# Performance work log

Hardware: AMD Instinct MI355X
Metric: run time of the kernel (lower is better)

The kernel has to match this reference:

```python
import jax, jax.numpy as jnp
import numpy as np
from jax import lax

N_QUBITS = 4


def _apply_ry(state, wire, theta):
    """Apply RY(theta) on `wire`. state: [N,2,2,2,2] real. theta: scalar or [N]."""
    theta = jnp.asarray(theta)
    if theta.ndim == 1:
        theta = theta.reshape(-1, 1, 1, 1)  # broadcast over remaining qubit axes
    s = jnp.moveaxis(state, 1 + wire, -1)
    c, sn = jnp.cos(theta / 2), jnp.sin(theta / 2)
    s0, s1 = s[..., 0], s[..., 1]
    s = jnp.stack([c * s0 - sn * s1, sn * s0 + c * s1], axis=-1)
    return jnp.moveaxis(s, -1, 1 + wire)


def _apply_cnot(state, ctrl, tgt):
    s = jnp.moveaxis(state, (1 + ctrl, 1 + tgt), (-2, -1))
    s = s.at[..., 1, :].set(s[..., 1, ::-1])
    return jnp.moveaxis(s, (-2, -1), (1 + ctrl, 1 + tgt))


def _quantum_filter(patches, angles):
    """patches: [N,4] rotation angles per qubit; returns PauliZ expectations [N,4]."""
    n = patches.shape[0]
    state = jnp.zeros((n, 2, 2, 2, 2), dtype=patches.dtype)
    state = state.at[:, 0, 0, 0, 0].set(1.0)  # |0000>
    # GeneralEncoder: RY(x_i) on wire i
    for w in range(N_QUBITS):
        state = _apply_ry(state, w, patches[:, w])
    # fixed 8-op random layer: 5 RY (learned angles) + 3 CNOTs
    state = _apply_ry(state, 0, angles[0])
    state = _apply_ry(state, 1, angles[1])
    state = _apply_cnot(state, 0, 1)
    state = _apply_ry(state, 2, angles[2])
    state = _apply_cnot(state, 1, 2)
    state = _apply_ry(state, 3, angles[3])
    state = _apply_cnot(state, 2, 3)
    state = _apply_ry(state, 0, angles[4])
    # MeasureAll(PauliZ): <Z_w> = sum probs * (+1/-1 on wire w)
    probs = state * state  # real amplitudes -> |psi|^2
    z = jnp.array([1.0, -1.0], dtype=patches.dtype)
    ez = [
        (probs * z.reshape((1,) + (1,) * w + (2,) + (1,) * (N_QUBITS - 1 - w))).sum(axis=(1, 2, 3, 4))
        for w in range(N_QUBITS)
    ]
    return jnp.stack(ez, axis=-1)  # [N,4]


def setup_inputs() -> dict:
    key = jax.random.key(0)
    ks = jax.random.split(key, 6)
    B = 4096
    return {
        "x": jax.random.normal(ks[0], (B, 1, 28, 28), dtype=jnp.float32),
        "conv_w": jax.random.normal(ks[1], (4, 1, 2, 2), dtype=jnp.float32) * 0.5,
        "conv_b": jax.random.normal(ks[2], (4,), dtype=jnp.float32) * 0.1,
        "angles": jax.random.normal(ks[3], (5,), dtype=jnp.float32) * np.pi,
        "fc_w": jax.random.normal(ks[4], (10, 4 * 14 * 14), dtype=jnp.float32) * 0.03,
        "fc_b": jax.random.normal(ks[5], (10,), dtype=jnp.float32) * 0.1,
    }


def reference(x, conv_w, conv_b, angles, fc_w, fc_b):
    # classical conv: kernel 2, stride 2 -> [B,4,14,14]
    y = lax.conv_general_dilated(
        x, conv_w, window_strides=(2, 2), padding="VALID",
        dimension_numbers=("NCHW", "OIHW", "NCHW"),
    ) + conv_b[None, :, None, None]
    B, C, H, W = y.shape
    patches = y.transpose(0, 2, 3, 1).reshape(B * H * W, C)  # [B*196, 4]
    feats = _quantum_filter(patches, angles)                  # [B*196, 4]
    feats = feats.reshape(B, H * W, C).transpose(0, 2, 1).reshape(B, -1)
    logits = feats @ fc_w.T + fc_b
    return jax.nn.log_softmax(logits, axis=-1)
```

## Files before the change

kernel.cpp:

```cpp
#include <hip/hip_runtime.h>
#include <math.h>

#define NP 196
#define FEAT 784


__device__ __forceinline__ void apply_cnot(float* s, const int mc, const int mt) {
#pragma unroll
    for (int i = 0; i < 16; ++i) {
        if ((i & mc) && !(i & mt)) {
            float t = s[i];
            s[i]      = s[i | mt];
            s[i | mt] = t;
        }
    }
}

__global__ void __launch_bounds__(256)
quanv_fused(const float* __restrict__ x,
            const float* __restrict__ cw,
            const float* __restrict__ cb,
            const float* __restrict__ ang,
            const float* __restrict__ W,
            const float* __restrict__ bias,
            float* __restrict__ out) {
    __shared__ float feats[FEAT];

    const int b   = blockIdx.x;
    const int tid = threadIdx.x;

    if (tid < NP) {
        const int i = tid / 14;
        const int j = tid - i * 14;

        const float* xp = x + b * 784 + (2 * i) * 28 + 2 * j;
        const float2 r0 = *(const float2*)(xp);
        const float2 r1 = *(const float2*)(xp + 28);

        float cs[4], sn[4];
#pragma unroll
        for (int c = 0; c < 4; ++c) {
            float th = cw[c * 4 + 0] * r0.x + cw[c * 4 + 1] * r0.y +
                       cw[c * 4 + 2] * r1.x + cw[c * 4 + 3] * r1.y +
                       (cb[c] + ang[c]);
            __sincosf(0.5f * th, &sn[c], &cs[c]);
        }

        float s[16];
        {
            float v00 = cs[0] * cs[1], v01 = cs[0] * sn[1];
            float v10 = sn[0] * cs[1], v11 = sn[0] * sn[1];
            float w00 = cs[2] * cs[3], w01 = cs[2] * sn[3];
            float w10 = sn[2] * cs[3], w11 = sn[2] * sn[3];
            s[ 0] = v00 * w00; s[ 1] = v00 * w01; s[ 2] = v00 * w10; s[ 3] = v00 * w11;
            s[ 4] = v01 * w00; s[ 5] = v01 * w01; s[ 6] = v01 * w10; s[ 7] = v01 * w11;
            s[ 8] = v10 * w00; s[ 9] = v10 * w01; s[10] = v10 * w10; s[11] = v10 * w11;
            s[12] = v11 * w00; s[13] = v11 * w01; s[14] = v11 * w10; s[15] = v11 * w11;
        }

        apply_cnot(s, 8, 4);
        apply_cnot(s, 4, 2);
        apply_cnot(s, 2, 1);

        float p[16];
#pragma unroll
        for (int idx = 0; idx < 16; ++idx) p[idx] = s[idx] * s[idx];

        float q[8], d[8], xx[8];
#pragma unroll
        for (int jj = 0; jj < 8; ++jj) {
            q[jj]  = p[jj] + p[jj + 8];
            d[jj]  = p[jj] - p[jj + 8];
            xx[jj] = s[jj] * s[jj + 8];
        }

        float A = q[0] + q[1], Bq = q[2] + q[3], C = q[4] + q[5], D = q[6] + q[7];
        float ez1 = (A + Bq) - (C + D);
        float ez2 = (A - Bq) + (C - D);
        float ez3 = (q[0] - q[1]) + (q[2] - q[3]) + (q[4] - q[5]) + (q[6] - q[7]);

        float Dsum = ((d[0] + d[1]) + (d[2] + d[3])) + ((d[4] + d[5]) + (d[6] + d[7]));
        float Xsum = ((xx[0] + xx[1]) + (xx[2] + xx[3])) + ((xx[4] + xx[5]) + (xx[6] + xx[7]));
        float ca4, sa4;
        __sincosf(ang[4], &sa4, &ca4);
        float ez0 = ca4 * Dsum - sa4 * (2.0f * Xsum);

        feats[0 * NP + tid] = ez0;
        feats[1 * NP + tid] = ez1;
        feats[2 * NP + tid] = ez2;
        feats[3 * NP + tid] = ez3;
    }

    __syncthreads();

    if (tid < 64) {
        const int lane = tid;
        float acc[10];
#pragma unroll
        for (int k = 0; k < 10; ++k) acc[k] = 0.f;

        for (int c = lane; c < NP; c += 64) {
            const float4 f = *(const float4*)&feats[c * 4];
            const float* wp = W + c * 4;
#pragma unroll
            for (int k = 0; k < 10; ++k) {
                const float4 w = *(const float4*)(wp + k * FEAT);
                acc[k] += fmaf(f.x, w.x, fmaf(f.y, w.y, fmaf(f.z, w.z, f.w * w.w)));
            }
        }

#pragma unroll
        for (int k = 0; k < 10; ++k) {
#pragma unroll
            for (int off = 32; off > 0; off >>= 1)
                acc[k] += __shfl_down(acc[k], off, 64);
        }

        if (lane == 0) {
            float l[10], m = -INFINITY;
#pragma unroll
            for (int k = 0; k < 10; ++k) {
                l[k] = acc[k] + bias[k];
                m = fmaxf(m, l[k]);
            }
            float ssum = 0.f;
#pragma unroll
            for (int k = 0; k < 10; ++k) ssum += __expf(l[k] - m);
            float ls = __logf(ssum) + m;
            float* o = out + b * 10;
#pragma unroll
            for (int k = 0; k < 10; ++k) o[k] = l[k] - ls;
        }
    }
}

extern "C" void kernel_launch(void* const* d_in, const int* in_sizes, int n_in,
                              void* d_out, int out_size, void* d_ws, size_t ws_size,
                              hipStream_t stream) {
    const float* x      = (const float*)d_in[0];
    const float* conv_w = (const float*)d_in[1];
    const float* conv_b = (const float*)d_in[2];
    const float* angles = (const float*)d_in[3];
    const float* fc_w   = (const float*)d_in[4];
    const float* fc_b   = (const float*)d_in[5];
    float* out = (float*)d_out;

    int B = in_sizes[0] / 784;
    quanv_fused<<<B, 256, 0, stream>>>(x, conv_w, conv_b, angles, fc_w, fc_b, out);
}
```

Measured before the change: 76.61 us.

## Process four images per block so all waves do quantum and FC work

Each 256-thread block now handles four images. All threads compute quantum features for 784 patches, with loads batched up front. Each of the four waves then runs the FC and log-softmax for one image. Previously 60 threads sat idle in the feature stage and three of four waves sat idle in the FC stage; the change raises utilization and cuts the grid size four-fold, at the cost of more registers and shared memory per block.

```diff
diff --git a/kernel.cpp b/kernel.cpp
--- a/kernel.cpp
+++ b/kernel.cpp
@@ -1,8 +1,9 @@
 #include <hip/hip_runtime.h>
 #include <math.h>
 
-#define NP 196
+#define NP   196
 #define FEAT 784
+#define IPB  4
 
 
 __device__ __forceinline__ void apply_cnot(float* s, const int mc, const int mt) {
@@ -16,121 +17,143 @@
     }
 }
 
-__global__ void __launch_bounds__(256)
+__global__ void __launch_bounds__(256, 4)
 quanv_fused(const float* __restrict__ x,
             const float* __restrict__ cw,
             const float* __restrict__ cb,
             const float* __restrict__ ang,
             const float* __restrict__ W,
             const float* __restrict__ bias,
-            float* __restrict__ out) {
-    __shared__ float feats[FEAT];
+            float* __restrict__ out,
+            const int B) {
+    __shared__ float feats[IPB][FEAT];
 
-    const int b   = blockIdx.x;
     const int tid = threadIdx.x;
+    const int b0  = blockIdx.x * IPB;
 
-    if (tid < NP) {
-        const int i = tid / 14;
-        const int j = tid - i * 14;
+    float2 r0v[4], r1v[4];
+#pragma unroll
+    for (int r = 0; r < 4; ++r) {
+        const int p = tid + 256 * r;
+        if (p < IPB * NP) {
+            const int im = p / NP;
+            const int k  = p - im * NP;
+            const int i  = k / 14;
+            const int j  = k - i * 14;
+            int img = b0 + im;
+            if (img >= B) img = B - 1;
+            const float* xp = x + img * 784 + (2 * i) * 28 + 2 * j;
+            r0v[r] = *(const float2*)(xp);
+            r1v[r] = *(const float2*)(xp + 28);
+        }
+    }
 
-        const float* xp = x + b * 784 + (2 * i) * 28 + 2 * j;
-        const float2 r0 = *(const float2*)(xp);
-        const float2 r1 = *(const float2*)(xp + 28);
+#pragma unroll
+    for (int r = 0; r < 4; ++r) {
+        const int p = tid + 256 * r;
+        if (p < IPB * NP) {
+            const int im = p / NP;
+            const int k  = p - im * NP;
+            const float2 r0 = r0v[r];
+            const float2 r1 = r1v[r];
 
-        float cs[4], sn[4];
+            float cs[4], sn[4];
 #pragma unroll
-        for (int c = 0; c < 4; ++c) {
-            float th = cw[c * 4 + 0] * r0.x + cw[c * 4 + 1] * r0.y +
-                       cw[c * 4 + 2] * r1.x + cw[c * 4 + 3] * r1.y +
-                       (cb[c] + ang[c]);
-            __sincosf(0.5f * th, &sn[c], &cs[c]);
+            for (int c = 0; c < 4; ++c) {
+                float th = cw[c * 4 + 0] * r0.x + cw[c * 4 + 1] * r0.y +
+                           cw[c * 4 + 2] * r1.x + cw[c * 4 + 3] * r1.y +
+                           (cb[c] + ang[c]);
+                __sincosf(0.5f * th, &sn[c], &cs[c]);
+            }
+
+            float s[16];
+            {
+                float v00 = cs[0] * cs[1], v01 = cs[0] * sn[1];
+                float v10 = sn[0] * cs[1], v11 = sn[0] * sn[1];
+                float w00 = cs[2] * cs[3], w01 = cs[2] * sn[3];
+                float w10 = sn[2] * cs[3], w11 = sn[2] * sn[3];
+                s[ 0] = v00 * w00; s[ 1] = v00 * w01; s[ 2] = v00 * w10; s[ 3] = v00 * w11;
+                s[ 4] = v01 * w00; s[ 5] = v01 * w01; s[ 6] = v01 * w10; s[ 7] = v01 * w11;
+                s[ 8] = v10 * w00; s[ 9] = v10 * w01; s[10] = v10 * w10; s[11] = v10 * w11;
+                s[12] = v11 * w00; s[13] = v11 * w01; s[14] = v11 * w10; s[15] = v11 * w11;
+            }
+
+            apply_cnot(s, 8, 4);
+            apply_cnot(s, 4, 2);
+            apply_cnot(s, 2, 1);
+
+            float pr[16];
+#pragma unroll
+            for (int idx = 0; idx < 16; ++idx) pr[idx] = s[idx] * s[idx];
+
+            float q[8], d[8], xx[8];
+#pragma unroll
+            for (int jj = 0; jj < 8; ++jj) {
+                q[jj]  = pr[jj] + pr[jj + 8];
+                d[jj]  = pr[jj] - pr[jj + 8];
+                xx[jj] = s[jj] * s[jj + 8];
+            }
+
+            float A = q[0] + q[1], Bq = q[2] + q[3], C = q[4] + q[5], D = q[6] + q[7];
+            float ez1 = (A + Bq) - (C + D);
+            float ez2 = (A - Bq) + (C - D);
+            float ez3 = (q[0] - q[1]) + (q[2] - q[3]) + (q[4] - q[5]) + (q[6] - q[7]);
+
+            float Dsum = ((d[0] + d[1]) + (d[2] + d[3])) + ((d[4] + d[5]) + (d[6] + d[7]));
+            float Xsum = ((xx[0] + xx[1]) + (xx[2] + xx[3])) + ((xx[4] + xx[5]) + (xx[6] + xx[7]));
+            float ca4, sa4;
+            __sincosf(ang[4], &sa4, &ca4);
+            float ez0 = ca4 * Dsum - sa4 * (2.0f * Xsum);
+
+            feats[im][0 * NP + k] = ez0;
+            feats[im][1 * NP + k] = ez1;
+            feats[im][2 * NP + k] = ez2;
+            feats[im][3 * NP + k] = ez3;
         }
-
-        float s[16];
-        {
-            float v00 = cs[0] * cs[1], v01 = cs[0] * sn[1];
-            float v10 = sn[0] * cs[1], v11 = sn[0] * sn[1];
-            float w00 = cs[2] * cs[3], w01 = cs[2] * sn[3];
-            float w10 = sn[2] * cs[3], w11 = sn[2] * sn[3];
-            s[ 0] = v00 * w00; s[ 1] = v00 * w01; s[ 2] = v00 * w10; s[ 3] = v00 * w11;
-            s[ 4] = v01 * w00; s[ 5] = v01 * w01; s[ 6] = v01 * w10; s[ 7] = v01 * w11;
-            s[ 8] = v10 * w00; s[ 9] = v10 * w01; s[10] = v10 * w10; s[11] = v10 * w11;
-            s[12] = v11 * w00; s[13] = v11 * w01; s[14] = v11 * w10; s[15] = v11 * w11;
-        }
-
-        apply_cnot(s, 8, 4);
-        apply_cnot(s, 4, 2);
-        apply_cnot(s, 2, 1);
-
-        float p[16];
-#pragma unroll
-        for (int idx = 0; idx < 16; ++idx) p[idx] = s[idx] * s[idx];
-
-        float q[8], d[8], xx[8];
-#pragma unroll
-        for (int jj = 0; jj < 8; ++jj) {
-            q[jj]  = p[jj] + p[jj + 8];
-            d[jj]  = p[jj] - p[jj + 8];
-            xx[jj] = s[jj] * s[jj + 8];
-        }
-
-        float A = q[0] + q[1], Bq = q[2] + q[3], C = q[4] + q[5], D = q[6] + q[7];
-        float ez1 = (A + Bq) - (C + D);
-        float ez2 = (A - Bq) + (C - D);
-        float ez3 = (q[0] - q[1]) + (q[2] - q[3]) + (q[4] - q[5]) + (q[6] - q[7]);
-
-        float Dsum = ((d[0] + d[1]) + (d[2] + d[3])) + ((d[4] + d[5]) + (d[6] + d[7]));
-        float Xsum = ((xx[0] + xx[1]) + (xx[2] + xx[3])) + ((xx[4] + xx[5]) + (xx[6] + xx[7]));
-        float ca4, sa4;
-        __sincosf(ang[4], &sa4, &ca4);
-        float ez0 = ca4 * Dsum - sa4 * (2.0f * Xsum);
-
-        feats[0 * NP + tid] = ez0;
-        feats[1 * NP + tid] = ez1;
-        feats[2 * NP + tid] = ez2;
-        feats[3 * NP + tid] = ez3;
     }
 
     __syncthreads();
 
-    if (tid < 64) {
-        const int lane = tid;
-        float acc[10];
+    const int wv   = tid >> 6;
+    const int lane = tid & 63;
+
+    float acc[10];
 #pragma unroll
-        for (int k = 0; k < 10; ++k) acc[k] = 0.f;
+    for (int k = 0; k < 10; ++k) acc[k] = 0.f;
 
-        for (int c = lane; c < NP; c += 64) {
-            const float4 f = *(const float4*)&feats[c * 4];
-            const float* wp = W + c * 4;
+    const float* fr = feats[wv];
+    for (int c = lane; c < NP; c += 64) {
+        const float4 f = *(const float4*)&fr[c * 4];
+        const float* wp = W + c * 4;
 #pragma unroll
-            for (int k = 0; k < 10; ++k) {
-                const float4 w = *(const float4*)(wp + k * FEAT);
-                acc[k] += fmaf(f.x, w.x, fmaf(f.y, w.y, fmaf(f.z, w.z, f.w * w.w)));
-            }
+        for (int k = 0; k < 10; ++k) {
+            const float4 w = *(const float4*)(wp + k * FEAT);
+            acc[k] += fmaf(f.x, w.x, fmaf(f.y, w.y, fmaf(f.z, w.z, f.w * w.w)));
         }
+    }
 
 #pragma unroll
+    for (int k = 0; k < 10; ++k) {
+#pragma unroll
+        for (int off = 32; off > 0; off >>= 1)
+            acc[k] += __shfl_down(acc[k], off, 64);
+    }
+
+    const int img = b0 + wv;
+    if (lane == 0 && img < B) {
+        float l[10], m = -INFINITY;
+#pragma unroll
         for (int k = 0; k < 10; ++k) {
+            l[k] = acc[k] + bias[k];
+            m = fmaxf(m, l[k]);
+        }
+        float ssum = 0.f;
 #pragma unroll
-            for (int off = 32; off > 0; off >>= 1)
-                acc[k] += __shfl_down(acc[k], off, 64);
-        }
-
-        if (lane == 0) {
-            float l[10], m = -INFINITY;
+        for (int k = 0; k < 10; ++k) ssum += __expf(l[k] - m);
+        float ls = __logf(ssum) + m;
+        float* o = out + img * 10;
 #pragma unroll
-            for (int k = 0; k < 10; ++k) {
-                l[k] = acc[k] + bias[k];
-                m = fmaxf(m, l[k]);
-            }
-            float ssum = 0.f;
-#pragma unroll
-            for (int k = 0; k < 10; ++k) ssum += __expf(l[k] - m);
-            float ls = __logf(ssum) + m;
-            float* o = out + b * 10;
-#pragma unroll
-            for (int k = 0; k < 10; ++k) o[k] = l[k] - ls;
-        }
+        for (int k = 0; k < 10; ++k) o[k] = l[k] - ls;
     }
 }
 
@@ -145,6 +168,7 @@
     const float* fc_b   = (const float*)d_in[5];
     float* out = (float*)d_out;
 
-    int B = in_sizes[0] / 784;
-    quanv_fused<<<B, 256, 0, stream>>>(x, conv_w, conv_b, angles, fc_w, fc_b, out);
+    int B  = in_sizes[0] / 784;
+    int nb = (B + IPB - 1) / IPB;
+    quanv_fused<<<nb, 256, 0, stream>>>(x, conv_w, conv_b, angles, fc_w, fc_b, out, B);
 }
```

Measured after the change: 76.57 us. About the same (-0.0%).
